# Performance work log

Measured on AMD Instinct MI355X. Metric: run time of the kernel, lower is better.

Reference implementation:

```python
import jax, jax.numpy as jnp
import numpy as np

VOCAB = 100000
EMB = 256
HID = 512
H2 = HID // 2
TAGS = 6
START = 3
STOP = 4
NEG = -10000.0
T = 4096


def setup_inputs() -> dict:
    key = jax.random.key(0)
    ks = jax.random.split(key, 16)
    s = 0.05
    trans = jax.random.normal(ks[12], (TAGS, TAGS), dtype=jnp.float32)
    trans = trans.at[START, :].set(NEG).at[:, STOP].set(NEG)
    return {
        "sentence": jax.random.randint(ks[0], (T,), 0, VOCAB, dtype=jnp.int32),
        "emb": jax.random.normal(ks[1], (VOCAB, EMB), dtype=jnp.float32) * s,
        "w_ih_f": jax.random.normal(ks[2], (4 * H2, EMB), dtype=jnp.float32) * s,
        "w_hh_f": jax.random.normal(ks[3], (4 * H2, H2), dtype=jnp.float32) * s,
        "b_ih_f": jax.random.normal(ks[4], (4 * H2,), dtype=jnp.float32) * s,
        "b_hh_f": jax.random.normal(ks[5], (4 * H2,), dtype=jnp.float32) * s,
        "w_ih_b": jax.random.normal(ks[6], (4 * H2, EMB), dtype=jnp.float32) * s,
        "w_hh_b": jax.random.normal(ks[7], (4 * H2, H2), dtype=jnp.float32) * s,
        "b_ih_b": jax.random.normal(ks[8], (4 * H2,), dtype=jnp.float32) * s,
        "b_hh_b": jax.random.normal(ks[9], (4 * H2,), dtype=jnp.float32) * s,
        "W_out": jax.random.normal(ks[10], (TAGS, HID), dtype=jnp.float32) * s,
        "b_out": jax.random.normal(ks[11], (TAGS,), dtype=jnp.float32) * s,
        "transitions": trans,
        "h0": jax.random.normal(ks[13], (2, H2), dtype=jnp.float32),
        "c0": jax.random.normal(ks[14], (2, H2), dtype=jnp.float32),
    }


def _lstm_dir(x, h0, c0, w_ih, w_hh, b_ih, b_hh, reverse):
    # x: (T, E); PyTorch LSTM gate order i, f, g, o
    def step(carry, xt):
        h, c = carry
        z = xt @ w_ih.T + b_ih + h @ w_hh.T + b_hh
        i, f, g, o = jnp.split(z, 4)
        i = jax.nn.sigmoid(i)
        f = jax.nn.sigmoid(f)
        g = jnp.tanh(g)
        o = jax.nn.sigmoid(o)
        c = f * c + i * g
        h = o * jnp.tanh(c)
        return (h, c), h

    _, hs = jax.lax.scan(step, (h0, c0), x, reverse=reverse)
    return hs  # (T, H2), time-aligned for both directions


def reference(sentence, emb, w_ih_f, w_hh_f, b_ih_f, b_hh_f,
              w_ih_b, w_hh_b, b_ih_b, b_hh_b, W_out, b_out,
              transitions, h0, c0):
    x = emb[sentence]  # (T, E)
    hf = _lstm_dir(x, h0[0], c0[0], w_ih_f, w_hh_f, b_ih_f, b_hh_f, False)
    hb = _lstm_dir(x, h0[1], c0[1], w_ih_b, w_hh_b, b_ih_b, b_hh_b, True)
    feats = jnp.concatenate([hf, hb], axis=-1) @ W_out.T + b_out  # (T, TAGS)

    init = jnp.full((TAGS,), NEG, dtype=feats.dtype).at[START].set(0.0)

    def vstep(fv, feat):
        tmp = transitions + fv[None, :]          # (to, from)
        bp = jnp.argmax(tmp, axis=1)             # best prev tag per next tag
        fv_new = tmp[jnp.arange(TAGS), bp] + feat
        return fv_new, bp

    fv, bptrs = jax.lax.scan(vstep, init, feats)  # bptrs: (T, TAGS)
    term = fv + transitions[STOP]
    best = jnp.argmax(term)
    score = term[best]

    def btstep(tag, bp):
        return bp[tag], tag

    _, path = jax.lax.scan(btstep, best, bptrs, reverse=True)  # (T,)
    return score, path
```

## Files before the change

kernel.cpp:

```cpp
#include <hip/hip_runtime.h>
#include <stdint.h>
#include <math.h>

#define T 4096
#define NTAGS 6
#define START_TAG 3
#define STOP_TAG 4
#define NEGV -10000.0f

__device__ __forceinline__ float sigm_fast(float z) {
  return 1.f / (1.f + __expf(-z));
}
__device__ __forceinline__ float tanh_fast(float z) {
  return 1.f - 2.f / (1.f + __expf(2.f * z));
}

typedef _Float16 half2v __attribute__((ext_vector_type(2)));
__device__ __forceinline__ float dot2acc(unsigned a, unsigned b, float c) {
  return __builtin_amdgcn_fdot2(__builtin_bit_cast(half2v, a),
                                __builtin_bit_cast(half2v, b), c, false);
}
__device__ __forceinline__ unsigned short f16b(float x) {
  _Float16 h = (_Float16)x;
  return __builtin_bit_cast(unsigned short, h);
}

__global__ __launch_bounds__(256) void k0_prep(
    const float* __restrict__ wf, const float* __restrict__ wb,
    const float* __restrict__ bif, const float* __restrict__ bhf,
    const float* __restrict__ bib, const float* __restrict__ bhb,
    float* __restrict__ wT, float* __restrict__ bias2) {
  int idx = blockIdx.x * 256 + threadIdx.x;
  int k = idx >> 11, col = idx & 2047;
  int d = col >> 10, g = col & 1023;
  const float* w = d ? wb : wf;
  wT[idx] = w[g * 256 + k];
  if (idx < 2048) bias2[idx] = d ? (bib[g] + bhb[g]) : (bif[g] + bhf[g]);
}

__global__ __launch_bounds__(256) void k1_zpre(
    const int* __restrict__ sent, const float* __restrict__ emb,
    const float* __restrict__ wT, const float* __restrict__ bias2,
    float* __restrict__ zpre) {
  int tb = blockIdx.x, cb = blockIdx.y;
  int tid = threadIdx.x;
  int col = cb * 256 + tid;
  int d = col >> 10, g = col & 1023;
  __shared__ float xs[32 * 256];
  int t0 = tb * 32;
  for (int r = 0; r < 32; r++) {
    int s = sent[t0 + r];
    xs[r * 256 + tid] = emb[(size_t)s * 256 + tid];
  }
  __syncthreads();
  float acc[32];
#pragma unroll
  for (int r = 0; r < 32; r++) acc[r] = 0.f;
  const float4* xs4 = (const float4*)xs;
  for (int kq = 0; kq < 64; kq++) {
    float w0 = wT[(4 * kq + 0) * 2048 + col];
    float w1 = wT[(4 * kq + 1) * 2048 + col];
    float w2 = wT[(4 * kq + 2) * 2048 + col];
    float w3 = wT[(4 * kq + 3) * 2048 + col];
#pragma unroll
    for (int r = 0; r < 32; r++) {
      float4 x4 = xs4[r * 64 + kq];
      acc[r] += w0 * x4.x + w1 * x4.y + w2 * x4.z + w3 * x4.w;
    }
  }
  float bb = bias2[col];
  for (int r = 0; r < 32; r++)
    zpre[((size_t)d * T + (t0 + r)) * 1024 + g] = acc[r] + bb;
}

__global__ __launch_bounds__(256) void k2_lstm(
    const float* __restrict__ zpre,
    const float* __restrict__ whf, const float* __restrict__ whb,
    const float* __restrict__ h0, const float* __restrict__ c0,
    float* h_all, unsigned long long* ring) {
  int w = blockIdx.x;
  int d = w >> 4, sub = w & 15;
  const float* w_hh = d ? whb : whf;
  int tid = threadIdx.x;
  int q = tid >> 6, lane = tid & 63;

  __shared__ uint4 wl4[32 * 64];
  __shared__ __align__(16) unsigned hq[4][32];
  __shared__ float z_part[4][64];

  {
    unsigned short* wlh = (unsigned short*)wl4;
    for (int idx = tid; idx < 64 * 256; idx += 256) {
      int r = idx >> 8, k = idx & 255;
      int gate = r >> 4, cell = r & 15;
      float wv = w_hh[(size_t)(gate * 256 + sub * 16 + cell) * 256 + k];
      int sq = k >> 6, sm = (k >> 3) & 7, sj = k & 7;
      wlh[((sq * 8 + sm) * 64 + r) * 8 + sj] = f16b(wv);
    }
  }
  if (lane < 32) {
    float f0 = h0[d * 256 + q * 64 + 2 * lane];
    float f1 = h0[d * 256 + q * 64 + 2 * lane + 1];
    hq[q][lane] = (unsigned)f16b(f0) | ((unsigned)f16b(f1) << 16);
  }
  float c = 0.f;
  if (tid < 16) c = c0[d * 256 + sub * 16 + tid];

  const float* zp_d = zpre + (size_t)d * T * 1024;
  float* h_d = h_all + (size_t)d * T * 256;
  unsigned long long* rg = ring + (size_t)d * 2 * 128;

  float zv4[4] = {0.f, 0.f, 0.f, 0.f};
  if (tid < 16) {
    int t0 = d ? (T - 1) : 0;
#pragma unroll
    for (int g = 0; g < 4; g++)
      zv4[g] = zp_d[(size_t)t0 * 1024 + g * 256 + sub * 16 + tid];
  }
  __syncthreads();

  for (int s = 0; s < T; s++) {
    int t = d ? (T - 1 - s) : s;
    float zn4[4] = {0.f, 0.f, 0.f, 0.f};
    if (tid < 16 && s + 1 < T) {
      int tn = d ? (t - 1) : (t + 1);
#pragma unroll
      for (int g = 0; g < 4; g++)
        zn4[g] = zp_d[(size_t)tn * 1024 + g * 256 + sub * 16 + tid];
    }

    if (s > 0 && lane < 32) {
      unsigned exp_tag = (unsigned)s;
      unsigned long long* addr = &rg[((s - 1) & 1) * 128 + q * 32 + lane];
      unsigned long long v;
      do {
        v = __hip_atomic_load(addr, __ATOMIC_RELAXED, __HIP_MEMORY_SCOPE_AGENT);
      } while ((unsigned)(v >> 32) != exp_tag);
      hq[q][lane] = (unsigned)v;
    }
    __builtin_amdgcn_wave_barrier();

    const uint4* hv = (const uint4*)hq[q];
    float acc = 0.f;
#pragma unroll
    for (int m = 0; m < 8; m++) {
      uint4 wv4 = wl4[(q * 8 + m) * 64 + lane];
      uint4 hv4 = hv[m];
      acc = dot2acc(wv4.x, hv4.x, acc);
      acc = dot2acc(wv4.y, hv4.y, acc);
      acc = dot2acc(wv4.z, hv4.z, acc);
      acc = dot2acc(wv4.w, hv4.w, acc);
    }
    z_part[q][lane] = acc;
    __syncthreads();

    if (tid < 16) {
      float a[4];
#pragma unroll
      for (int g = 0; g < 4; g++) {
        int r = g * 16 + tid;
        float z = z_part[0][r] + z_part[1][r] + z_part[2][r] + z_part[3][r]
                + zv4[g];
        a[g] = (g == 2) ? tanh_fast(z) : sigm_fast(z);
      }
      c = a[1] * c + a[0] * a[2];
      float hvl = a[3] * tanh_fast(c);
      h_d[(size_t)t * 256 + sub * 16 + tid] = hvl;
      float hn = __shfl_down(hvl, 1);
      if ((tid & 1) == 0) {
        unsigned h2 = (unsigned)f16b(hvl) | ((unsigned)f16b(hn) << 16);
        __hip_atomic_store(&rg[(s & 1) * 128 + sub * 8 + (tid >> 1)],
                           ((unsigned long long)(unsigned)(s + 1) << 32) | h2,
                           __ATOMIC_RELAXED, __HIP_MEMORY_SCOPE_AGENT);
      }
#pragma unroll
      for (int g = 0; g < 4; g++) zv4[g] = zn4[g];
    }
    __syncthreads();
  }
}

__global__ __launch_bounds__(64) void k3_feats(
    const float* __restrict__ h_all, const float* __restrict__ Wout,
    const float* __restrict__ bout, float* __restrict__ feats) {
  int t = blockIdx.x;
  int j = threadIdx.x;
  const float* hf = h_all + (size_t)t * 256;
  const float* hb = h_all + (size_t)T * 256 + (size_t)t * 256;
  float s[6];
#pragma unroll
  for (int g = 0; g < 6; g++) s[g] = 0.f;
#pragma unroll
  for (int m = 0; m < 4; m++) {
    float a = hf[j + 64 * m];
#pragma unroll
    for (int g = 0; g < 6; g++) s[g] += a * Wout[g * 512 + j + 64 * m];
  }
#pragma unroll
  for (int m = 0; m < 4; m++) {
    float b = hb[j + 64 * m];
#pragma unroll
    for (int g = 0; g < 6; g++) s[g] += b * Wout[g * 512 + 256 + j + 64 * m];
  }
#pragma unroll
  for (int g = 0; g < 6; g++) {
#pragma unroll
    for (int off = 32; off >= 1; off >>= 1) s[g] += __shfl_xor(s[g], off);
  }
  if (j < 6) feats[(size_t)t * 6 + j] = s[j] + bout[j];
}

__global__ __launch_bounds__(64) void k4_viterbi(
    const float* __restrict__ feats, const float* __restrict__ trans,
    float* __restrict__ out) {
  __shared__ unsigned char bp_lds[T * 8];
  __shared__ float fbuf[2][64 * 6];
  int lane = threadIdx.x;

  float tr[6];
#pragma unroll
  for (int f = 0; f < 6; f++) tr[f] = (lane < 6) ? trans[lane * 6 + f] : 0.f;
  float fv = (lane == START_TAG) ? 0.f : NEGV;

  for (int idx = lane; idx < 384; idx += 64) fbuf[0][idx] = feats[idx];

  for (int cch = 0; cch < 64; cch++) {
    float pf[6];
    if (cch + 1 < 64) {
#pragma unroll
      for (int m = 0; m < 6; m++)
        pf[m] = feats[(cch + 1) * 384 + lane + 64 * m];
    }
    const float* fb = fbuf[cch & 1];
    for (int j = 0; j < 64; j++) {
      int t = cch * 64 + j;
      float best = -3.4e38f;
      int bi = 0;
#pragma unroll
      for (int f = 0; f < 6; f++) {
        float v = __shfl(fv, f) + tr[f];
        if (v > best) { best = v; bi = f; }
      }
      float nfv = best + fb[j * 6 + (lane < 6 ? lane : 0)];
      if (lane < 6) {
        fv = nfv;
        bp_lds[t * 8 + lane] = (unsigned char)bi;
      }
    }
    if (cch + 1 < 64) {
#pragma unroll
      for (int m = 0; m < 6; m++)
        fbuf[(cch + 1) & 1][lane + 64 * m] = pf[m];
    }
  }

  float term = (lane < 6) ? (fv + trans[STOP_TAG * 6 + lane]) : -3.4e38f;
  float bestv = -3.4e38f;
  int bestt = 0;
#pragma unroll
  for (int f = 0; f < 6; f++) {
    float v = __shfl(term, f);
    if (v > bestv) { bestv = v; bestt = f; }
  }
  if (lane == 0) out[0] = bestv;

  unsigned int ident = 0;
#pragma unroll
  for (int i = 0; i < 6; i++) ident |= (unsigned)i << (3 * i);

  unsigned int p = ident;
  int base = lane * 64;
  for (int j2 = 0; j2 < 64; j2++) {
    const unsigned int* bw = (const unsigned int*)&bp_lds[(base + j2) * 8];
    unsigned int lo = bw[0], hi = bw[1];
    unsigned int mw = (lo & 7) | (((lo >> 8) & 7) << 3) | (((lo >> 16) & 7) << 6)
                    | (((lo >> 24) & 7) << 9) | ((hi & 7) << 12)
                    | (((hi >> 8) & 7) << 15);
    unsigned int np = 0;
#pragma unroll
    for (int i = 0; i < 6; i++) {
      unsigned int b = (mw >> (3 * i)) & 7;
      np |= ((p >> (3 * b)) & 7) << (3 * i);
    }
    p = np;
  }
  unsigned int suf = p;
#pragma unroll
  for (int off = 1; off < 64; off <<= 1) {
    unsigned int other = __shfl_down(suf, off);
    if (lane + off < 64) {
      unsigned int ns = 0;
#pragma unroll
      for (int i = 0; i < 6; i++) {
        unsigned int b = (other >> (3 * i)) & 7;
        ns |= ((suf >> (3 * b)) & 7) << (3 * i);
      }
      suf = ns;
    }
  }
  unsigned int tail = __shfl_down(suf, 1);
  if (lane == 63) tail = ident;
  unsigned int cur = tail;
  for (int j2 = 63; j2 >= 0; j2--) {
    int t = base + j2;
    out[1 + t] = (float)((cur >> (3 * bestt)) & 7);
    const unsigned int* bw = (const unsigned int*)&bp_lds[t * 8];
    unsigned int lo = bw[0], hi = bw[1];
    unsigned int mw = (lo & 7) | (((lo >> 8) & 7) << 3) | (((lo >> 16) & 7) << 6)
                    | (((lo >> 24) & 7) << 9) | ((hi & 7) << 12)
                    | (((hi >> 8) & 7) << 15);
    unsigned int nc = 0;
#pragma unroll
    for (int i = 0; i < 6; i++) {
      unsigned int b = (cur >> (3 * i)) & 7;
      nc |= ((mw >> (3 * b)) & 7) << (3 * i);
    }
    cur = nc;
  }
}

extern "C" void kernel_launch(void* const* d_in, const int* in_sizes, int n_in,
                              void* d_out, int out_size, void* d_ws, size_t ws_size,
                              hipStream_t stream) {
  const int*   sent  = (const int*)d_in[0];
  const float* emb   = (const float*)d_in[1];
  const float* wihf  = (const float*)d_in[2];
  const float* whhf  = (const float*)d_in[3];
  const float* bihf  = (const float*)d_in[4];
  const float* bhhf  = (const float*)d_in[5];
  const float* wihb  = (const float*)d_in[6];
  const float* whhb  = (const float*)d_in[7];
  const float* bihb  = (const float*)d_in[8];
  const float* bhhb  = (const float*)d_in[9];
  const float* Wout  = (const float*)d_in[10];
  const float* bout  = (const float*)d_in[11];
  const float* trans = (const float*)d_in[12];
  const float* h0    = (const float*)d_in[13];
  const float* c0    = (const float*)d_in[14];
  float* out = (float*)d_out;

  char* ws = (char*)d_ws;
  float*              zpre  = (float*)(ws + 0);
  float*              h_all = (float*)(ws + 33554432);
  float*              wT    = (float*)(ws + 41943040);
  float*              bias2 = (float*)(ws + 44040192);
  float*              feats = (float*)(ws + 44048384);
  unsigned long long* ring  = (unsigned long long*)(ws + 44146688);

  k0_prep<<<2048, 256, 0, stream>>>(wihf, wihb, bihf, bhhf, bihb, bhhb, wT, bias2);
  dim3 g1(128, 8);
  k1_zpre<<<g1, 256, 0, stream>>>(sent, emb, wT, bias2, zpre);
  k2_lstm<<<32, 256, 0, stream>>>(zpre, whhf, whhb, h0, c0, h_all, ring);
  k3_feats<<<4096, 64, 0, stream>>>(h_all, Wout, bout, feats);
  k4_viterbi<<<1, 64, 0, stream>>>(feats, trans, out);
}
```

Before: 6.478 ms.

## Halve LSTM recurrence blocks and add sc0 fast-path ring with atomic fallback

The recurrent LSTM kernel now uses 16 working blocks instead of 32. Each block owns 32 cells per direction and does twice the dot-product work per step. It launches 128 blocks and keeps only every eighth, apparently to place the workers on separate XCDs/L2s. The handoff of h between blocks now writes two rings: a fast one through inline-asm loads and stores with the sc0 cache hint, and the original agent-scope atomic ring as a fallback that is polled after four failed fast attempts. The zpre prefetch is moved after the spin-wait. The aim is to cut per-step cross-block sync latency and the number of participants. The cost is more compute per block and reliance on cache-coherence behaviour of the sc0 hint.

Result: slower. 7.641 ms (+18.0%).

```diff
diff --git a/kernel.cpp b/kernel.cpp
--- a/kernel.cpp
+++ b/kernel.cpp
@@ -23,6 +23,19 @@
 __device__ __forceinline__ unsigned short f16b(float x) {
   _Float16 h = (_Float16)x;
   return __builtin_bit_cast(unsigned short, h);
+}
+
+__device__ __forceinline__ unsigned long long load_l2(
+    const unsigned long long* p) {
+  unsigned long long v;
+  asm volatile("global_load_dwordx2 %0, %1, off sc0\n\ts_waitcnt vmcnt(0)"
+               : "=v"(v) : "v"(p) : "memory");
+  return v;
+}
+__device__ __forceinline__ void store_l2(unsigned long long* p,
+                                         unsigned long long v) {
+  asm volatile("global_store_dwordx2 %0, %1, off sc0"
+               :: "v"(p), "v"(v) : "memory");
 }
 
 __global__ __launch_bounds__(256) void k0_prep(
@@ -77,25 +90,26 @@
     const float* __restrict__ zpre,
     const float* __restrict__ whf, const float* __restrict__ whb,
     const float* __restrict__ h0, const float* __restrict__ c0,
-    float* h_all, unsigned long long* ring) {
-  int w = blockIdx.x;
-  int d = w >> 4, sub = w & 15;
+    float* h_all, unsigned long long* fastr, unsigned long long* slowr) {
+  if (blockIdx.x % 8 != 0) return;
+  int slot = blockIdx.x / 8;
+  int d = slot >> 3, sub = slot & 7;
   const float* w_hh = d ? whb : whf;
   int tid = threadIdx.x;
   int q = tid >> 6, lane = tid & 63;
 
-  __shared__ uint4 wl4[32 * 64];
+  __shared__ uint4 wl4[32 * 128];
   __shared__ __align__(16) unsigned hq[4][32];
-  __shared__ float z_part[4][64];
+  __shared__ float z_part[4][128];
 
   {
     unsigned short* wlh = (unsigned short*)wl4;
-    for (int idx = tid; idx < 64 * 256; idx += 256) {
+    for (int idx = tid; idx < 128 * 256; idx += 256) {
       int r = idx >> 8, k = idx & 255;
-      int gate = r >> 4, cell = r & 15;
-      float wv = w_hh[(size_t)(gate * 256 + sub * 16 + cell) * 256 + k];
+      int gate = r >> 5, cell = r & 31;
+      float wv = w_hh[(size_t)(gate * 256 + sub * 32 + cell) * 256 + k];
       int sq = k >> 6, sm = (k >> 3) & 7, sj = k & 7;
-      wlh[((sq * 8 + sm) * 64 + r) * 8 + sj] = f16b(wv);
+      wlh[((sq * 8 + sm) * 128 + r) * 8 + sj] = f16b(wv);
     }
   }
   if (lane < 32) {
@@ -104,74 +118,91 @@
     hq[q][lane] = (unsigned)f16b(f0) | ((unsigned)f16b(f1) << 16);
   }
   float c = 0.f;
-  if (tid < 16) c = c0[d * 256 + sub * 16 + tid];
+  if (tid < 32) c = c0[d * 256 + sub * 32 + tid];
 
   const float* zp_d = zpre + (size_t)d * T * 1024;
   float* h_d = h_all + (size_t)d * T * 256;
-  unsigned long long* rg = ring + (size_t)d * 2 * 128;
+  unsigned long long* f_rg = fastr + (size_t)d * 256;
+  unsigned long long* s_rg = slowr + (size_t)d * 256;
 
   float zv4[4] = {0.f, 0.f, 0.f, 0.f};
-  if (tid < 16) {
+  if (tid < 32) {
     int t0 = d ? (T - 1) : 0;
 #pragma unroll
     for (int g = 0; g < 4; g++)
-      zv4[g] = zp_d[(size_t)t0 * 1024 + g * 256 + sub * 16 + tid];
+      zv4[g] = zp_d[(size_t)t0 * 1024 + g * 256 + sub * 32 + tid];
   }
   __syncthreads();
 
   for (int s = 0; s < T; s++) {
     int t = d ? (T - 1 - s) : s;
-    float zn4[4] = {0.f, 0.f, 0.f, 0.f};
-    if (tid < 16 && s + 1 < T) {
-      int tn = d ? (t - 1) : (t + 1);
-#pragma unroll
-      for (int g = 0; g < 4; g++)
-        zn4[g] = zp_d[(size_t)tn * 1024 + g * 256 + sub * 16 + tid];
-    }
 
     if (s > 0 && lane < 32) {
       unsigned exp_tag = (unsigned)s;
-      unsigned long long* addr = &rg[((s - 1) & 1) * 128 + q * 32 + lane];
+      int ridx = ((s - 1) & 1) * 128 + q * 32 + lane;
+      const unsigned long long* fa = &f_rg[ridx];
       unsigned long long v;
-      do {
-        v = __hip_atomic_load(addr, __ATOMIC_RELAXED, __HIP_MEMORY_SCOPE_AGENT);
-      } while ((unsigned)(v >> 32) != exp_tag);
+      for (;;) {
+        bool got = false;
+#pragma unroll 1
+        for (int it = 0; it < 4; ++it) {
+          v = load_l2(fa);
+          if ((unsigned)(v >> 32) == exp_tag) { got = true; break; }
+        }
+        if (got) break;
+        v = __hip_atomic_load(&s_rg[ridx], __ATOMIC_RELAXED,
+                              __HIP_MEMORY_SCOPE_AGENT);
+        if ((unsigned)(v >> 32) == exp_tag) break;
+      }
       hq[q][lane] = (unsigned)v;
     }
     __builtin_amdgcn_wave_barrier();
 
-    const uint4* hv = (const uint4*)hq[q];
-    float acc = 0.f;
+    float zn4[4] = {0.f, 0.f, 0.f, 0.f};
+    if (tid < 32 && s + 1 < T) {
+      int tn = d ? (t - 1) : (t + 1);
+#pragma unroll
+      for (int g = 0; g < 4; g++)
+        zn4[g] = zp_d[(size_t)tn * 1024 + g * 256 + sub * 32 + tid];
+    }
+
+    const uint4* hq4 = (const uint4*)(&hq[q][0]);
+    float accA = 0.f, accB = 0.f;
 #pragma unroll
     for (int m = 0; m < 8; m++) {
-      uint4 wv4 = wl4[(q * 8 + m) * 64 + lane];
-      uint4 hv4 = hv[m];
-      acc = dot2acc(wv4.x, hv4.x, acc);
-      acc = dot2acc(wv4.y, hv4.y, acc);
-      acc = dot2acc(wv4.z, hv4.z, acc);
-      acc = dot2acc(wv4.w, hv4.w, acc);
-    }
-    z_part[q][lane] = acc;
+      uint4 hv4 = hq4[m];
+      uint4 wA = wl4[(q * 8 + m) * 128 + lane];
+      uint4 wB = wl4[(q * 8 + m) * 128 + 64 + lane];
+      accA = dot2acc(wA.x, hv4.x, accA); accA = dot2acc(wA.y, hv4.y, accA);
+      accA = dot2acc(wA.z, hv4.z, accA); accA = dot2acc(wA.w, hv4.w, accA);
+      accB = dot2acc(wB.x, hv4.x, accB); accB = dot2acc(wB.y, hv4.y, accB);
+      accB = dot2acc(wB.z, hv4.z, accB); accB = dot2acc(wB.w, hv4.w, accB);
+    }
+    z_part[q][lane] = accA;
+    z_part[q][64 + lane] = accB;
     __syncthreads();
 
-    if (tid < 16) {
+    if (tid < 32) {
       float a[4];
 #pragma unroll
       for (int g = 0; g < 4; g++) {
-        int r = g * 16 + tid;
+        int r = g * 32 + tid;
         float z = z_part[0][r] + z_part[1][r] + z_part[2][r] + z_part[3][r]
                 + zv4[g];
         a[g] = (g == 2) ? tanh_fast(z) : sigm_fast(z);
       }
       c = a[1] * c + a[0] * a[2];
       float hvl = a[3] * tanh_fast(c);
-      h_d[(size_t)t * 256 + sub * 16 + tid] = hvl;
+      h_d[(size_t)t * 256 + sub * 32 + tid] = hvl;
       float hn = __shfl_down(hvl, 1);
       if ((tid & 1) == 0) {
         unsigned h2 = (unsigned)f16b(hvl) | ((unsigned)f16b(hn) << 16);
-        __hip_atomic_store(&rg[(s & 1) * 128 + sub * 8 + (tid >> 1)],
-                           ((unsigned long long)(unsigned)(s + 1) << 32) | h2,
-                           __ATOMIC_RELAXED, __HIP_MEMORY_SCOPE_AGENT);
+        unsigned long long pkt =
+            ((unsigned long long)(unsigned)(s + 1) << 32) | h2;
+        int widx = (s & 1) * 128 + sub * 16 + (tid >> 1);
+        store_l2(&f_rg[widx], pkt);
+        __hip_atomic_store(&s_rg[widx], pkt, __ATOMIC_RELAXED,
+                           __HIP_MEMORY_SCOPE_AGENT);
       }
 #pragma unroll
       for (int g = 0; g < 4; g++) zv4[g] = zn4[g];
@@ -345,12 +376,13 @@
   float*              wT    = (float*)(ws + 41943040);
   float*              bias2 = (float*)(ws + 44040192);
   float*              feats = (float*)(ws + 44048384);
-  unsigned long long* ring  = (unsigned long long*)(ws + 44146688);
+  unsigned long long* fastr = (unsigned long long*)(ws + 44146688);
+  unsigned long long* slowr = (unsigned long long*)(ws + 44150784);
 
   k0_prep<<<2048, 256, 0, stream>>>(wihf, wihb, bihf, bhhf, bihb, bhhb, wT, bias2);
   dim3 g1(128, 8);
   k1_zpre<<<g1, 256, 0, stream>>>(sent, emb, wT, bias2, zpre);
-  k2_lstm<<<32, 256, 0, stream>>>(zpre, whhf, whhb, h0, c0, h_all, ring);
+  k2_lstm<<<128, 256, 0, stream>>>(zpre, whhf, whhb, h0, c0, h_all, fastr, slowr);
   k3_feats<<<4096, 64, 0, stream>>>(h_all, Wout, bout, feats);
   k4_viterbi<<<1, 64, 0, stream>>>(feats, trans, out);
 }
```
